# Optimization experiments

Measured on AMD Instinct MI355X. Metric: run time of the kernel, lower is better.

Reference implementation:

```python
import jax, jax.numpy as jnp
import numpy as np

N_NODES = 100000
N_EDGES = 3200000
IN_DIM = 62
OUT_DIM = 16
EDGE_DIM = 2


def setup_inputs() -> dict:
    key = jax.random.key(0)
    ks = jax.random.split(key, 8)
    h = jax.random.normal(ks[0], (N_NODES, IN_DIM), dtype=jnp.float32)
    e = jax.random.normal(ks[1], (N_EDGES, EDGE_DIM), dtype=jnp.float32)
    src = jax.random.randint(ks[2], (N_EDGES,), 0, N_NODES, dtype=jnp.int32)
    dst = jax.random.randint(ks[3], (N_EDGES,), 0, N_NODES, dtype=jnp.int32)
    # xavier-normal-ish scaled weights
    W_fc = jax.random.normal(ks[4], (OUT_DIM, IN_DIM), dtype=jnp.float32) * 0.2
    W_attn = jax.random.normal(ks[5], (1, 2 * OUT_DIM + EDGE_DIM), dtype=jnp.float32) * 0.2
    W_edge = jax.random.normal(ks[6], (EDGE_DIM, EDGE_DIM), dtype=jnp.float32) * 0.5
    W_e2n = jax.random.normal(ks[7], (OUT_DIM, EDGE_DIM), dtype=jnp.float32) * 0.5
    return {"h": h, "e": e, "src": src, "dst": dst, "W_fc": W_fc,
            "W_attn": W_attn, "W_edge": W_edge, "W_e2n": W_e2n}


def _agat_forward(h, e, src, dst, W_fc, W_attn, W_edge, W_e2n):
    n = h.shape[0]
    d = W_fc.shape[0]
    z = h @ W_fc.T                      # [N, D]
    ex = e @ W_edge.T                   # [E, edge_dim]
    # attn_fc([z_src, z_dst, ex]) split into per-part projections
    Wa_src = W_attn[:, :d]              # [1, D]
    Wa_dst = W_attn[:, d:2 * d]         # [1, D]
    Wa_e = W_attn[:, 2 * d:]            # [1, edge_dim]
    a_src = (z @ Wa_src.T)[:, 0]        # [N] per-node, gathered per-edge
    a_dst = (z @ Wa_dst.T)[:, 0]        # [N]
    a = a_src[src] + a_dst[dst] + (ex @ Wa_e.T)[:, 0]   # [E]
    e_att = jax.nn.leaky_relu(a, negative_slope=0.01)    # [E]
    # segment softmax over incoming edges of each dst node
    m = jax.ops.segment_max(e_att, dst, num_segments=n)  # [N]
    w = jnp.exp(e_att - m[dst])                           # [E]
    denom = jax.ops.segment_sum(w, dst, num_segments=n)   # [N]
    attn = w / denom[dst]                                  # [E]
    # message = z_src + ez; aggregated as attn-weighted sum (matches
    # sum(attn*z) + sum(attn*ez) in reduce_func)
    ez = ex @ W_e2n.T                                      # [E, D]
    msg = attn[:, None] * (z[src] + ez)                    # [E, D]
    return jax.ops.segment_sum(msg, dst, num_segments=n)   # [N, D]


def reference(h, e, src, dst, W_fc, W_attn, W_edge, W_e2n):
    return _agat_forward(h, e, src, dst, W_fc, W_attn, W_edge, W_e2n)
```

## Files before the change

### kernel.cpp

```cpp
#include <hip/hip_runtime.h>
#include <hip/hip_fp16.h>

#define N_NODES 100000
#define N_EDGES 3200000
#define IN_DIM  62
#define OUT_DIM 16

#define EBC    4096
#define NEB    ((N_EDGES + EBC - 1) / EBC)
#define NPB    ((N_NODES + 1023) / 1024)
#define NBUCK  ((N_NODES + 63) / 64)
#define CAPL   4096

typedef int nat_i2 __attribute__((ext_vector_type(2)));

__global__ __launch_bounds__(1024) void proj_append_kernel(
    const float* __restrict__ h,
    const float* __restrict__ W_fc,
    const float* __restrict__ W_attn,
    const float* __restrict__ e,
    const int*   __restrict__ src,
    const int*   __restrict__ dst,
    __half* __restrict__ zh,
    float* __restrict__ a_src_arr,
    float* __restrict__ a_dst_arr,
    int*   __restrict__ cursor,
    nat_i2* __restrict__ records,
    int cap)
{
    __shared__ int  cnt[NBUCK];
    __shared__ int  pfx[NBUCK];
    __shared__ int  combo[NBUCK];
    __shared__ int2 pay[EBC];
    __shared__ unsigned short pbkt[EBC];
    __shared__ int  wsum[16];

    int tid = threadIdx.x;

    if (blockIdx.x < NPB) {
        int i = blockIdx.x * 1024 + tid;
        if (i >= N_NODES) return;

        float acc[OUT_DIM];
#pragma unroll
        for (int j = 0; j < OUT_DIM; ++j) acc[j] = 0.f;

        const float2* __restrict__ hr = (const float2*)(h + (size_t)i * IN_DIM);
#pragma unroll
        for (int kk = 0; kk < IN_DIM / 2; ++kk) {
            float2 hv = hr[kk];
#pragma unroll
            for (int j = 0; j < OUT_DIM; ++j) {
                acc[j] += hv.x * W_fc[j * IN_DIM + 2 * kk]
                        + hv.y * W_fc[j * IN_DIM + 2 * kk + 1];
            }
        }

        float asrc = 0.f, adst = 0.f;
#pragma unroll
        for (int j = 0; j < OUT_DIM; ++j) {
            asrc += acc[j] * W_attn[j];
            adst += acc[j] * W_attn[OUT_DIM + j];
        }

        union { __half hx[16]; uint4 q[2]; } u;
#pragma unroll
        for (int j = 0; j < OUT_DIM; ++j) u.hx[j] = __float2half(acc[j]);
        uint4* __restrict__ zrow = (uint4*)(zh + (size_t)i * OUT_DIM);
        zrow[0] = u.q[0];
        zrow[1] = u.q[1];

        a_src_arr[i] = asrc;
        a_dst_arr[i] = adst;
        return;
    }

    int be = blockIdx.x - NPB;
    long ebase = (long)be * EBC;
    int chunk_n = (int)min((long)EBC, (long)N_EDGES - ebase);

    for (int t = tid; t < NBUCK; t += 1024) cnt[t] = 0;

    int dv0 = -1, dv1 = -1, dv2 = -1, dv3 = -1;
    int sv0 = 0, sv1 = 0, sv2 = 0, sv3 = 0;
    float2 ev0, ev1, ev2, ev3;
    {
        int p;
        p = tid;          if (p < chunk_n) { long eid = ebase + p; dv0 = dst[eid]; sv0 = src[eid]; ev0 = ((const float2*)e)[eid]; }
        p = tid + 1024;   if (p < chunk_n) { long eid = ebase + p; dv1 = dst[eid]; sv1 = src[eid]; ev1 = ((const float2*)e)[eid]; }
        p = tid + 2048;   if (p < chunk_n) { long eid = ebase + p; dv2 = dst[eid]; sv2 = src[eid]; ev2 = ((const float2*)e)[eid]; }
        p = tid + 3072;   if (p < chunk_n) { long eid = ebase + p; dv3 = dst[eid]; sv3 = src[eid]; ev3 = ((const float2*)e)[eid]; }
    }
    __syncthreads();

    if (dv0 >= 0) atomicAdd(&cnt[dv0 >> 6], 1);
    if (dv1 >= 0) atomicAdd(&cnt[dv1 >> 6], 1);
    if (dv2 >= 0) atomicAdd(&cnt[dv2 >> 6], 1);
    if (dv3 >= 0) atomicAdd(&cnt[dv3 >> 6], 1);
    __syncthreads();

    int b0 = 2 * tid, b1 = b0 + 1;
    int c0 = (b0 < NBUCK) ? cnt[b0] : 0;
    int c1 = (b1 < NBUCK) ? cnt[b1] : 0;
    int ts = c0 + c1;
    {
        int lane = tid & 63, wid = tid >> 6;
        int x = ts;
#pragma unroll
        for (int off = 1; off < 64; off <<= 1) {
            int y = __shfl_up(x, off, 64);
            if (lane >= off) x += y;
        }
        if (lane == 63) wsum[wid] = x;
        __syncthreads();
        if (wid == 0) {
            int v = (lane < 16) ? wsum[lane] : 0;
#pragma unroll
            for (int off = 1; off < 16; off <<= 1) {
                int y = __shfl_up(v, off, 64);
                if (lane >= off) v += y;
            }
            if (lane < 16) wsum[lane] = v;
        }
        __syncthreads();
        int texcl = x - ts + (wid ? wsum[wid - 1] : 0);
        if (b0 < NBUCK) pfx[b0] = texcl;
        if (b1 < NBUCK) pfx[b1] = texcl + c0;
    }
    __syncthreads();

    for (int t = tid; t < NBUCK; t += 1024) {
        int v = cnt[t];
        if (v) {
            int gbase = atomicAdd(&cursor[t], v);
            combo[t] = t * cap + gbase - pfx[t];
        }
        cnt[t] = 0;
    }
    __syncthreads();

#define PLACE(dv, sv, ev)                                                  \
    if (dv >= 0) {                                                         \
        int b = dv >> 6;                                                   \
        union { __half2 h2; int i; } uu;                                   \
        uu.h2.x = __float2half(ev.x);                                      \
        uu.h2.y = __float2half(ev.y);                                      \
        int r = atomicAdd(&cnt[b], 1);                                     \
        int q = pfx[b] + r;                                                \
        pay[q]  = make_int2(uu.i, sv | ((dv & 63) << 17));                 \
        pbkt[q] = (unsigned short)b;                                       \
    }
    PLACE(dv0, sv0, ev0)
    PLACE(dv1, sv1, ev1)
    PLACE(dv2, sv2, ev2)
    PLACE(dv3, sv3, ev3)
#undef PLACE
    __syncthreads();

    for (int p = tid; p < chunk_n; p += 1024) {
        int2 v = pay[p];
        int bb = pbkt[p];
        int pos = combo[bb] + p;
        if (pos < (bb + 1) * cap) {
            nat_i2 vv; vv.x = v.x; vv.y = v.y;
            __builtin_nontemporal_store(vv, records + pos);
        }
    }
}

__global__ __launch_bounds__(1024) void bucket_gather_kernel(
    const int*    __restrict__ cursor,
    const nat_i2* __restrict__ records,
    const __half* __restrict__ zh,
    const float*  __restrict__ a_src_arr,
    const float*  __restrict__ a_dst_arr,
    const float*  __restrict__ W_attn,
    const float*  __restrict__ W_edge,
    const float*  __restrict__ W_e2n,
    float* __restrict__ out, int cap)
{
    __shared__ int2 rec[CAPL];
    __shared__ unsigned short inv[CAPL];
    __shared__ unsigned int exb[CAPL];
    __shared__ int hist[64], pfx[64], cur[64];
    __shared__ float adst_l[64];

    int b   = blockIdx.x;
    int tid = threadIdx.x;
    long lo = (long)b * cap;
    int n   = cursor[b];
    int nl  = n < cap ? n : cap;
    if (nl > CAPL) nl = CAPL;

    if (tid < 64) {
        hist[tid] = 0; cur[tid] = 0;
        int node = (b << 6) + tid;
        adst_l[tid] = (node < N_NODES) ? a_dst_arr[node] : 0.f;
    }
    __syncthreads();

    float we00 = W_edge[0], we01 = W_edge[1], we10 = W_edge[2], we11 = W_edge[3];
    float wa0  = W_attn[2 * OUT_DIM], wa1 = W_attn[2 * OUT_DIM + 1];

    int ld0 = -1, ld1 = -1, ld2 = -1, ld3 = -1;
#define EDGEW(J, LD)                                                        \
    {                                                                       \
        int k = tid + (J) * 1024;                                           \
        if (k < nl) {                                                       \
            nat_i2 r = __builtin_nontemporal_load(records + lo + k);        \
            int s  = r.y & 0x1FFFF;                                         \
            LD     = (r.y >> 17) & 63;                                      \
            union { int i; __half2 h2; } ue; ue.i = r.x;                    \
            float e0 = __low2float(ue.h2), e1 = __high2float(ue.h2);        \
            float ex0 = e0 * we00 + e1 * we01;                              \
            float ex1 = e0 * we10 + e1 * we11;                              \
            float a = a_src_arr[s] + adst_l[LD] + ex0 * wa0 + ex1 * wa1;    \
            float ea = (a > 0.f) ? a : 0.01f * a;                           \
            float w  = __expf(ea);                                          \
            rec[k] = make_int2(__float_as_int(w), r.y);                     \
            union { unsigned int i; __half2 h2; } up;                       \
            up.h2.x = __float2half(ex0);                                    \
            up.h2.y = __float2half(ex1);                                    \
            exb[k] = up.i;                                                  \
            atomicAdd(&hist[LD], 1);                                        \
        }                                                                   \
    }
    EDGEW(0, ld0) EDGEW(1, ld1) EDGEW(2, ld2) EDGEW(3, ld3)
#undef EDGEW
    __syncthreads();

    if (tid < 64) pfx[tid] = hist[tid];
    __syncthreads();
    for (int off = 1; off < 64; off <<= 1) {
        int t = 0;
        if (tid < 64 && tid >= off) t = pfx[tid - off];
        __syncthreads();
        if (tid < 64) pfx[tid] += t;
        __syncthreads();
    }
    if (tid < 64) pfx[tid] -= hist[tid];
    __syncthreads();

#define INVW(J, LD)                                                         \
    if (LD >= 0) {                                                          \
        int k = tid + (J) * 1024;                                           \
        int r = atomicAdd(&cur[LD], 1);                                     \
        inv[pfx[LD] + r] = (unsigned short)k;                               \
    }
    INVW(0, ld0) INVW(1, ld1) INVW(2, ld2) INVW(3, ld3)
#undef INVW
    __syncthreads();

    int ld   = tid >> 4;
    int lane = tid & 15;
    int node = (b << 6) + ld;
    if (node >= N_NODES) return;

    int m    = hist[ld];
    int base = pfx[ld];

    float acc0 = 0.f, acc1 = 0.f, accw0 = 0.f, accw1 = 0.f;
    float ax00 = 0.f, ax01 = 0.f, ax10 = 0.f, ax11 = 0.f;

    int i = 0;
    for (; i + 1 < m; i += 2) {
        int k0 = inv[base + i];
        int k1 = inv[base + i + 1];
        int2 r0 = rec[k0];
        int2 r1 = rec[k1];
        float w0 = __int_as_float(r0.x);
        float w1 = __int_as_float(r1.x);
        int s0 = r0.y & 0x1FFFF;
        int s1 = r1.y & 0x1FFFF;
        union { unsigned int i; __half2 h2; } x0, x1;
        x0.i = exb[k0];
        x1.i = exb[k1];

        float zv0 = __half2float(zh[s0 * OUT_DIM + lane]);
        float zv1 = __half2float(zh[s1 * OUT_DIM + lane]);

        acc0  += w0 * zv0;                 acc1  += w1 * zv1;
        accw0 += w0;                       accw1 += w1;
        ax00  += w0 * __low2float(x0.h2);  ax01  += w1 * __low2float(x1.h2);
        ax10  += w0 * __high2float(x0.h2); ax11  += w1 * __high2float(x1.h2);
    }
    if (i < m) {
        int k0 = inv[base + i];
        int2 r0 = rec[k0];
        float w0 = __int_as_float(r0.x);
        int s0 = r0.y & 0x1FFFF;
        union { unsigned int i; __half2 h2; } x0;
        x0.i = exb[k0];
        float zv0 = __half2float(zh[s0 * OUT_DIM + lane]);
        acc0  += w0 * zv0;
        accw0 += w0;
        ax00  += w0 * __low2float(x0.h2);
        ax10  += w0 * __high2float(x0.h2);
    }

    float acc  = acc0 + acc1;
    float accw = accw0 + accw1;
    float ax0  = ax00 + ax01;
    float ax1  = ax10 + ax11;

    float ez   = ax0 * W_e2n[2 * lane] + ax1 * W_e2n[2 * lane + 1];
    float invw = (accw != 0.f) ? (1.f / accw) : 0.f;
    out[(size_t)node * OUT_DIM + lane] = (acc + ez) * invw;
}


__global__ __launch_bounds__(256) void node_proj_fb_kernel(
    const float* __restrict__ h,
    const float* __restrict__ W_fc,
    const float* __restrict__ W_attn,
    float* __restrict__ z,
    float* __restrict__ a_src_arr,
    float* __restrict__ a_dst_arr,
    float* __restrict__ denom,
    float* __restrict__ out)
{
    int i = blockIdx.x * blockDim.x + threadIdx.x;
    if (i >= N_NODES) return;

    float acc[OUT_DIM];
#pragma unroll
    for (int j = 0; j < OUT_DIM; ++j) acc[j] = 0.f;

    const float2* __restrict__ hr = (const float2*)(h + (size_t)i * IN_DIM);
#pragma unroll
    for (int kk = 0; kk < IN_DIM / 2; ++kk) {
        float2 hv = hr[kk];
#pragma unroll
        for (int j = 0; j < OUT_DIM; ++j) {
            acc[j] += hv.x * W_fc[j * IN_DIM + 2 * kk]
                    + hv.y * W_fc[j * IN_DIM + 2 * kk + 1];
        }
    }

    float asrc = 0.f, adst = 0.f;
#pragma unroll
    for (int j = 0; j < OUT_DIM; ++j) {
        asrc += acc[j] * W_attn[j];
        adst += acc[j] * W_attn[OUT_DIM + j];
    }

    float4* __restrict__ zrow = (float4*)(z + (size_t)i * OUT_DIM);
    zrow[0] = make_float4(acc[0],  acc[1],  acc[2],  acc[3]);
    zrow[1] = make_float4(acc[4],  acc[5],  acc[6],  acc[7]);
    zrow[2] = make_float4(acc[8],  acc[9],  acc[10], acc[11]);
    zrow[3] = make_float4(acc[12], acc[13], acc[14], acc[15]);

    a_src_arr[i] = asrc;
    a_dst_arr[i] = adst;
    denom[i] = 0.f;

    float4 z4 = make_float4(0.f, 0.f, 0.f, 0.f);
    float4* __restrict__ orow = (float4*)(out + (size_t)i * OUT_DIM);
    orow[0] = z4; orow[1] = z4; orow[2] = z4; orow[3] = z4;
}

__global__ __launch_bounds__(256) void edge_kernel(
    const float* __restrict__ e,
    const int*   __restrict__ src,
    const int*   __restrict__ dst,
    const float* __restrict__ W_attn,
    const float* __restrict__ W_edge,
    const float* __restrict__ W_e2n,
    const float* __restrict__ z,
    const float* __restrict__ a_src_arr,
    const float* __restrict__ a_dst_arr,
    float* __restrict__ denom,
    float* __restrict__ out)
{
    int eid = blockIdx.x * blockDim.x + threadIdx.x;
    if (eid >= N_EDGES) return;

    int s = src[eid];
    int d = dst[eid];

    float2 ev = ((const float2*)e)[eid];
    float ex0 = ev.x * W_edge[0] + ev.y * W_edge[1];
    float ex1 = ev.x * W_edge[2] + ev.y * W_edge[3];

    float a = a_src_arr[s] + a_dst_arr[d]
            + ex0 * W_attn[2 * OUT_DIM] + ex1 * W_attn[2 * OUT_DIM + 1];
    float ea = (a > 0.f) ? a : 0.01f * a;
    float w  = __expf(ea);

    unsafeAtomicAdd(denom + d, w);

    const float4* __restrict__ zrow = (const float4*)(z + (size_t)s * OUT_DIM);
    float4 z0 = zrow[0], z1 = zrow[1], z2 = zrow[2], z3 = zrow[3];

    float* __restrict__ orow = out + (size_t)d * OUT_DIM;
    float zs[OUT_DIM] = { z0.x, z0.y, z0.z, z0.w,
                          z1.x, z1.y, z1.z, z1.w,
                          z2.x, z2.y, z2.z, z2.w,
                          z3.x, z3.y, z3.z, z3.w };
#pragma unroll
    for (int j = 0; j < OUT_DIM; ++j) {
        float ez = ex0 * W_e2n[2 * j] + ex1 * W_e2n[2 * j + 1];
        unsafeAtomicAdd(orow + j, w * (zs[j] + ez));
    }
}

__global__ __launch_bounds__(256) void normalize_kernel(
    float* __restrict__ out, const float* __restrict__ denom)
{
    int tid = blockIdx.x * blockDim.x + threadIdx.x;
    const int total = N_NODES * OUT_DIM / 4;
    if (tid >= total) return;
    int n = tid >> 2;
    float dn = denom[n];
    float inv = (dn != 0.f) ? (1.f / dn) : 0.f;
    float4 v = ((float4*)out)[tid];
    v.x *= inv; v.y *= inv; v.z *= inv; v.w *= inv;
    ((float4*)out)[tid] = v;
}

extern "C" void kernel_launch(void* const* d_in, const int* in_sizes, int n_in,
                              void* d_out, int out_size, void* d_ws, size_t ws_size,
                              hipStream_t stream)
{
    const float* h      = (const float*)d_in[0];
    const float* e      = (const float*)d_in[1];
    const int*   src    = (const int*)  d_in[2];
    const int*   dst    = (const int*)  d_in[3];
    const float* W_fc   = (const float*)d_in[4];
    const float* W_attn = (const float*)d_in[5];
    const float* W_edge = (const float*)d_in[6];
    const float* W_e2n  = (const float*)d_in[7];
    float* out = (float*)d_out;

    char* ws = (char*)d_ws;

    size_t off = 0;
    __half* zh        = (__half*)(ws + off); off += (size_t)N_NODES * OUT_DIM * 2;
    float*  a_src_arr = (float*) (ws + off); off += (size_t)N_NODES * 4;
    float*  a_dst_arr = (float*) (ws + off); off += (size_t)N_NODES * 4;
    int*    cursor    = (int*)   (ws + off); off += (size_t)NBUCK * 4;
    size_t rec_off = (off + 255) & ~(size_t)255;

    int cap = 0;
    if      (ws_size >= rec_off + (size_t)NBUCK * 4096 * 8) cap = 4096;
    else if (ws_size >= rec_off + (size_t)NBUCK * 3072 * 8) cap = 3072;
    else if (ws_size >= rec_off + (size_t)NBUCK * 2560 * 8) cap = 2560;
    else if (ws_size >= rec_off + (size_t)NBUCK * 2304 * 8) cap = 2304;

    if (cap) {
        nat_i2* records = (nat_i2*)(ws + rec_off);

        hipMemsetAsync(cursor, 0, (size_t)NBUCK * sizeof(int), stream);

        proj_append_kernel<<<NPB + NEB, 1024, 0, stream>>>(
            h, W_fc, W_attn, e, src, dst,
            zh, a_src_arr, a_dst_arr, cursor, records, cap);

        bucket_gather_kernel<<<NBUCK, 1024, 0, stream>>>(
            cursor, records, zh, a_src_arr, a_dst_arr,
            W_attn, W_edge, W_e2n, out, cap);
    } else {
        size_t foff = 0;
        float* z     = (float*)(ws + foff); foff += (size_t)N_NODES * OUT_DIM * 4;
        float* asrc  = (float*)(ws + foff); foff += (size_t)N_NODES * 4;
        float* adst  = (float*)(ws + foff); foff += (size_t)N_NODES * 4;
        float* denom = (float*)(ws + foff); foff += (size_t)N_NODES * 4;

        node_proj_fb_kernel<<<(N_NODES + 255) / 256, 256, 0, stream>>>(
            h, W_fc, W_attn, z, asrc, adst, denom, out);

        edge_kernel<<<(N_EDGES + 255) / 256, 256, 0, stream>>>(
            e, src, dst, W_attn, W_edge, W_e2n, z, asrc, adst, denom, out);

        normalize_kernel<<<(N_NODES * OUT_DIM / 4 + 255) / 256, 256, 0, stream>>>(
            out, denom);
    }
}
```

Measured before the change: 224.3 us.

## Enlarge edge chunks, pad global bucket cursors, overlap cursor atomics with scan

Raises edges per block from 4096 to 6144 (six per thread, in a loop), so fewer blocks each issue the per-bucket global cursor atomics. Cursor counters are padded to a 16-int stride so each bucket's atomic lands on its own 64-byte line, reducing contention between neighbouring buckets. The global atomicAdd for bucket offsets is now issued before the block prefix scan and folded into it, which removes a separate loop and a barrier. In exchange, each bucket gets more records per chunk and the edge values held in registers grow by half, which may lower occupancy.

```diff
diff --git a/kernel.cpp b/kernel.cpp
--- a/kernel.cpp
+++ b/kernel.cpp
@@ -6,11 +6,13 @@
 #define IN_DIM  62
 #define OUT_DIM 16
 
-#define EBC    4096
+#define EBC    6144
+#define EPT    (EBC / 1024)
 #define NEB    ((N_EDGES + EBC - 1) / EBC)
 #define NPB    ((N_NODES + 1023) / 1024)
 #define NBUCK  ((N_NODES + 63) / 64)
 #define CAPL   4096
+#define CSTR   16
 
 typedef int nat_i2 __attribute__((ext_vector_type(2)));
 
@@ -79,29 +81,37 @@
     long ebase = (long)be * EBC;
     int chunk_n = (int)min((long)EBC, (long)N_EDGES - ebase);
 
+    int dv[EPT], sv[EPT];
+    float2 ev[EPT];
+#pragma unroll
+    for (int j = 0; j < EPT; ++j) {
+        int p = tid + j * 1024;
+        dv[j] = -1;
+        if (p < chunk_n) {
+            long eid = ebase + p;
+            dv[j] = dst[eid];
+            sv[j] = src[eid];
+            ev[j] = ((const float2*)e)[eid];
+        }
+    }
+
     for (int t = tid; t < NBUCK; t += 1024) cnt[t] = 0;
-
-    int dv0 = -1, dv1 = -1, dv2 = -1, dv3 = -1;
-    int sv0 = 0, sv1 = 0, sv2 = 0, sv3 = 0;
-    float2 ev0, ev1, ev2, ev3;
-    {
-        int p;
-        p = tid;          if (p < chunk_n) { long eid = ebase + p; dv0 = dst[eid]; sv0 = src[eid]; ev0 = ((const float2*)e)[eid]; }
-        p = tid + 1024;   if (p < chunk_n) { long eid = ebase + p; dv1 = dst[eid]; sv1 = src[eid]; ev1 = ((const float2*)e)[eid]; }
-        p = tid + 2048;   if (p < chunk_n) { long eid = ebase + p; dv2 = dst[eid]; sv2 = src[eid]; ev2 = ((const float2*)e)[eid]; }
-        p = tid + 3072;   if (p < chunk_n) { long eid = ebase + p; dv3 = dst[eid]; sv3 = src[eid]; ev3 = ((const float2*)e)[eid]; }
-    }
-    __syncthreads();
-
-    if (dv0 >= 0) atomicAdd(&cnt[dv0 >> 6], 1);
-    if (dv1 >= 0) atomicAdd(&cnt[dv1 >> 6], 1);
-    if (dv2 >= 0) atomicAdd(&cnt[dv2 >> 6], 1);
-    if (dv3 >= 0) atomicAdd(&cnt[dv3 >> 6], 1);
+    __syncthreads();
+
+#pragma unroll
+    for (int j = 0; j < EPT; ++j)
+        if (dv[j] >= 0) atomicAdd(&cnt[dv[j] >> 6], 1);
     __syncthreads();
 
     int b0 = 2 * tid, b1 = b0 + 1;
     int c0 = (b0 < NBUCK) ? cnt[b0] : 0;
     int c1 = (b1 < NBUCK) ? cnt[b1] : 0;
+    if (b0 < NBUCK) cnt[b0] = 0;
+    if (b1 < NBUCK) cnt[b1] = 0;
+    int gb0 = 0, gb1 = 0;
+    if (c0) gb0 = atomicAdd(&cursor[b0 * CSTR], c0);
+    if (c1) gb1 = atomicAdd(&cursor[b1 * CSTR], c1);
+
     int ts = c0 + c1;
     {
         int lane = tid & 63, wid = tid >> 6;
@@ -124,37 +134,24 @@
         }
         __syncthreads();
         int texcl = x - ts + (wid ? wsum[wid - 1] : 0);
-        if (b0 < NBUCK) pfx[b0] = texcl;
-        if (b1 < NBUCK) pfx[b1] = texcl + c0;
-    }
-    __syncthreads();
-
-    for (int t = tid; t < NBUCK; t += 1024) {
-        int v = cnt[t];
-        if (v) {
-            int gbase = atomicAdd(&cursor[t], v);
-            combo[t] = t * cap + gbase - pfx[t];
-        }
-        cnt[t] = 0;
-    }
-    __syncthreads();
-
-#define PLACE(dv, sv, ev)                                                  \
-    if (dv >= 0) {                                                         \
-        int b = dv >> 6;                                                   \
-        union { __half2 h2; int i; } uu;                                   \
-        uu.h2.x = __float2half(ev.x);                                      \
-        uu.h2.y = __float2half(ev.y);                                      \
-        int r = atomicAdd(&cnt[b], 1);                                     \
-        int q = pfx[b] + r;                                                \
-        pay[q]  = make_int2(uu.i, sv | ((dv & 63) << 17));                 \
-        pbkt[q] = (unsigned short)b;                                       \
-    }
-    PLACE(dv0, sv0, ev0)
-    PLACE(dv1, sv1, ev1)
-    PLACE(dv2, sv2, ev2)
-    PLACE(dv3, sv3, ev3)
-#undef PLACE
+        if (b0 < NBUCK) { pfx[b0] = texcl;      combo[b0] = b0 * cap + gb0 - texcl; }
+        if (b1 < NBUCK) { pfx[b1] = texcl + c0; combo[b1] = b1 * cap + gb1 - (texcl + c0); }
+    }
+    __syncthreads();
+
+#pragma unroll
+    for (int j = 0; j < EPT; ++j) {
+        if (dv[j] >= 0) {
+            int b = dv[j] >> 6;
+            union { __half2 h2; int i; } uu;
+            uu.h2.x = __float2half(ev[j].x);
+            uu.h2.y = __float2half(ev[j].y);
+            int r = atomicAdd(&cnt[b], 1);
+            int q = pfx[b] + r;
+            pay[q]  = make_int2(uu.i, sv[j] | ((dv[j] & 63) << 17));
+            pbkt[q] = (unsigned short)b;
+        }
+    }
     __syncthreads();
 
     for (int p = tid; p < chunk_n; p += 1024) {
@@ -188,7 +185,7 @@
     int b   = blockIdx.x;
     int tid = threadIdx.x;
     long lo = (long)b * cap;
-    int n   = cursor[b];
+    int n   = cursor[b * CSTR];
     int nl  = n < cap ? n : cap;
     if (nl > CAPL) nl = CAPL;
 
@@ -438,7 +435,7 @@
     __half* zh        = (__half*)(ws + off); off += (size_t)N_NODES * OUT_DIM * 2;
     float*  a_src_arr = (float*) (ws + off); off += (size_t)N_NODES * 4;
     float*  a_dst_arr = (float*) (ws + off); off += (size_t)N_NODES * 4;
-    int*    cursor    = (int*)   (ws + off); off += (size_t)NBUCK * 4;
+    int*    cursor    = (int*)   (ws + off); off += (size_t)NBUCK * CSTR * 4;
     size_t rec_off = (off + 255) & ~(size_t)255;
 
     int cap = 0;
@@ -450,7 +447,7 @@
     if (cap) {
         nat_i2* records = (nat_i2*)(ws + rec_off);
 
-        hipMemsetAsync(cursor, 0, (size_t)NBUCK * sizeof(int), stream);
+        hipMemsetAsync(cursor, 0, (size_t)NBUCK * CSTR * sizeof(int), stream);
 
         proj_append_kernel<<<NPB + NEB, 1024, 0, stream>>>(
             h, W_fc, W_attn, e, src, dst,
```

New measurement: 220.5 us. No clear change (-1.7%).
